# Kernel optimization log

Hardware: AMD Instinct MI355X
Metric: run time of the kernel (lower is better)

The kernel has to match this reference:

```python
import jax, jax.numpy as jnp
import numpy as np

T, B, H, L = 2048, 4096, 4, 3

def setup_inputs() -> dict:
    key = jax.random.key(0)
    ks = jax.random.split(key, 6)
    scale = 1.0 / np.sqrt(H)  # PyTorch nn.RNN init range ~U(-1/sqrt(H), 1/sqrt(H)); use normal*scale for simplicity
    return {
        "x": jax.random.normal(ks[0], (T, B, H), dtype=jnp.float32),
        "h": jax.random.normal(ks[1], (L, B, H), dtype=jnp.float32),
        "Wih": jax.random.normal(ks[2], (L, H, H), dtype=jnp.float32) * scale,
        "Whh": jax.random.normal(ks[3], (L, H, H), dtype=jnp.float32) * scale,
        "bih": jax.random.normal(ks[4], (L, H), dtype=jnp.float32) * scale,
        "bhh": jax.random.normal(ks[5], (L, H), dtype=jnp.float32) * scale,
    }

def _rnn_layer(x, h0, W_ih, W_hh, b_ih, b_hh):
    # x: (T, B, H); h0: (B, H). Vanilla tanh RNN, matching torch nn.RNN layer math:
    # h_t = tanh(x_t @ W_ih^T + b_ih + h_{t-1} @ W_hh^T + b_hh)
    b = b_ih + b_hh
    def step(h, xt):
        h_new = jnp.tanh(xt @ W_ih.T + h @ W_hh.T + b)
        return h_new, h_new
    _, ys = jax.lax.scan(step, h0, x)
    return ys  # (T, B, H)

def reference(x, h, Wih, Whh, bih, bhh):
    out = x
    for l in range(Wih.shape[0]):  # small fixed layer count (3)
        out = _rnn_layer(out, h[l], Wih[l], Whh[l], bih[l], bhh[l])
    return out  # (T, B, H): all-timestep outputs of last layer
```

## Files before the change

### kernel.cpp

```cpp
#include <hip/hip_runtime.h>

#define TSTEPS 2048
#define BATCH  4096
#define HID    4
#define STRIDE (BATCH*HID)
#define CH     32
#define NCHUNK (TSTEPS/CH)
#define NPH    69

#define QB(v,k) __int_as_float(__builtin_amdgcn_update_dpp( \
    0, __float_as_int(v), (k)*0x55, 0xF, 0xF, true))

__device__ __forceinline__ float fast_exp2(float x) {
#if __has_builtin(__builtin_amdgcn_exp2f)
  return __builtin_amdgcn_exp2f(x);
#else
  return exp2f(x);
#endif
}
__device__ __forceinline__ float fast_rcp(float x) {
#if __has_builtin(__builtin_amdgcn_rcpf)
  return __builtin_amdgcn_rcpf(x);
#else
  return 1.0f / x;
#endif
}

__device__ __forceinline__ void xload(float* ldst, const float* gsrc) {
  __builtin_amdgcn_global_load_lds(
      (const __attribute__((address_space(1))) void*)gsrc,
      (__attribute__((address_space(3))) void*)ldst, 4, 0, 0);
}

__global__ __launch_bounds__(256) void rnn_pipe4(
    const float* __restrict__ X,
    const float* __restrict__ H0,
    const float* __restrict__ Wih,
    const float* __restrict__ Whh,
    const float* __restrict__ bih,
    const float* __restrict__ bhh,
    float* __restrict__ Y)
{
  const int lane = threadIdx.x & 63;
  const int wid  = threadIdx.x >> 6;
  const int g    = blockIdx.x * 64 + lane;
  const int j    = g & 3;
  const float K  = 2.8853900817779268f;

  __shared__ float iface[3][2][CH][64];
  __shared__ float xbuf[3][CH][64];

  float whp[HID], win[HID], cbn = 0.0f, r = 0.0f;
  {
    const int Lt = wid - 1;
    const int Ln = wid;
    if (wid >= 1) {
#pragma unroll
      for (int k = 0; k < HID; ++k)
        whp[k] = -2.0f * K * Whh[(Lt*HID + j)*HID + k];
      r = 0.5f * (1.0f - H0[Lt*STRIDE + g]);
    }
    if (wid <= 2) {
      float wsum = 0.0f;
#pragma unroll
      for (int k = 0; k < HID; ++k) {
        win[k] = K * Wih[(Ln*HID + j)*HID + k];
        wsum  += Whh[(Ln*HID + j)*HID + k];
      }
      cbn = K * (bih[Ln*HID + j] + bhh[Ln*HID + j] + wsum);
    }
  }

  const float* __restrict__ xp = X + g;

  if (wid == 0) {
    __builtin_amdgcn_sched_barrier(0);
    asm volatile("s_waitcnt vmcnt(0)" ::: "memory");
#pragma unroll
    for (int u = 0; u < CH; ++u)
      xload(&xbuf[0][u][0], xp + (size_t)(0*CH + u) * STRIDE);
#pragma unroll
    for (int u = 0; u < CH; ++u)
      xload(&xbuf[1][u][0], xp + (size_t)(1*CH + u) * STRIDE);
  }

  auto phase = [&](int p, int slot) {
    if (wid == 0) {
      if (p <= NCHUNK - 1) {
        const int par = p & 1;
        asm volatile("s_waitcnt vmcnt(32)" ::: "memory");
        __builtin_amdgcn_sched_barrier(0);
        float xv[CH];
#pragma unroll
        for (int u = 0; u < CH; ++u) xv[u] = xbuf[slot][u][lane];
        __builtin_amdgcn_sched_barrier(0);
#pragma unroll
        for (int u = 0; u < CH; ++u) {
          float a = cbn;
          a = fmaf(QB(xv[u], 0), win[0], a);
          a = fmaf(QB(xv[u], 1), win[1], a);
          a = fmaf(QB(xv[u], 2), win[2], a);
          a = fmaf(QB(xv[u], 3), win[3], a);
          iface[0][par][u][lane] = a;
        }
#pragma unroll
        for (int u = 0; u < CH; ++u) {
          int tn = (p + 2) * CH + u;
          if (tn > TSTEPS - 1) tn = TSTEPS - 1;
          xload(&xbuf[(slot+2)%3][u][0], xp + (size_t)tn * STRIDE);
        }
      }
    } else {
      const int m = p - wid;
      if (m >= 0 && m <= NCHUNK - 1) {
        const int par = m & 1;
        float av[CH];
#pragma unroll
        for (int u = 0; u < CH; ++u) av[u] = iface[wid-1][par][u][lane];
        __builtin_amdgcn_sched_barrier(0);
        if (wid <= 2) {
#pragma unroll
          for (int u = 0; u < CH; ++u) {
            float t0 = fmaf(QB(r, 0), whp[0], av[u]);
            float t1 =      QB(r, 1) * whp[1];
            t0 = fmaf(QB(r, 2), whp[2], t0);
            t1 = fmaf(QB(r, 3), whp[3], t1);
            float e = fast_exp2(t0 + t1);
            r = fast_rcp(e + 1.0f);
            float h = fmaf(-2.0f, r, 1.0f);
            float a = cbn;
            a = fmaf(QB(h, 0), win[0], a);
            a = fmaf(QB(h, 1), win[1], a);
            a = fmaf(QB(h, 2), win[2], a);
            a = fmaf(QB(h, 3), win[3], a);
            iface[wid][par][u][lane] = a;
          }
        } else {
          const int base = m * CH;
#pragma unroll
          for (int u = 0; u < CH; ++u) {
            float t0 = fmaf(QB(r, 0), whp[0], av[u]);
            float t1 =      QB(r, 1) * whp[1];
            t0 = fmaf(QB(r, 2), whp[2], t0);
            t1 = fmaf(QB(r, 3), whp[3], t1);
            float e = fast_exp2(t0 + t1);
            r = fast_rcp(e + 1.0f);
            Y[(size_t)(base + u) * STRIDE + g] = fmaf(-2.0f, r, 1.0f);
          }
        }
      }
    }

    __builtin_amdgcn_sched_barrier(0);
    asm volatile("s_waitcnt lgkmcnt(0)" ::: "memory");
    __builtin_amdgcn_s_barrier();
    __builtin_amdgcn_sched_barrier(0);
  };

  for (int p = 0; p < NPH; p += 3) {
    phase(p + 0, 0);
    phase(p + 1, 1);
    phase(p + 2, 2);
  }

  if (wid == 0) asm volatile("s_waitcnt vmcnt(0)" ::: "memory");
}

extern "C" void kernel_launch(void* const* d_in, const int* in_sizes, int n_in,
                              void* d_out, int out_size, void* d_ws, size_t ws_size,
                              hipStream_t stream) {
  const float* X   = (const float*)d_in[0];
  const float* H0  = (const float*)d_in[1];
  const float* Wih = (const float*)d_in[2];
  const float* Whh = (const float*)d_in[3];
  const float* bih = (const float*)d_in[4];
  const float* bhh = (const float*)d_in[5];
  float* Y = (float*)d_out;

  rnn_pipe4<<<dim3(STRIDE / 64), dim3(256), 0, stream>>>(X, H0, Wih, Whh, bih, bhh, Y);
}
```

Before: 115.0 us.

## Double block to two wave groups and fold tanh affine into next-layer projection

Each block now holds two independent 4-wave pipelines, each covering 64 batch-hidden columns, and uses 512 threads, halving the grid. The middle layers skip computing h = 1 - 2r. They project r directly with pre-scaled weights (-2K*Wih), and the Wih row sum is folded into the bias. That projection is shifted one step so it reuses the DPP broadcasts already needed for the recurrent term. The intent is to shorten the serial per-step dependency chain and share barrier and launch overhead, at the cost of doubled LDS per block and possibly lower occupancy.

```diff
diff --git a/kernel.cpp b/kernel.cpp
--- a/kernel.cpp
+++ b/kernel.cpp
@@ -32,7 +32,7 @@
       (__attribute__((address_space(3))) void*)ldst, 4, 0, 0);
 }
 
-__global__ __launch_bounds__(256) void rnn_pipe4(
+__global__ __launch_bounds__(512) void rnn_pipe8(
     const float* __restrict__ X,
     const float* __restrict__ H0,
     const float* __restrict__ Wih,
@@ -42,30 +42,42 @@
     float* __restrict__ Y)
 {
   const int lane = threadIdx.x & 63;
-  const int wid  = threadIdx.x >> 6;
-  const int g    = blockIdx.x * 64 + lane;
+  const int w    = threadIdx.x >> 6;
+  const int role = w & 3;
+  const int grp  = w >> 2;
+  const int g    = blockIdx.x * 128 + grp * 64 + lane;
   const int j    = g & 3;
   const float K  = 2.8853900817779268f;
 
-  __shared__ float iface[3][2][CH][64];
-  __shared__ float xbuf[3][CH][64];
-
-  float whp[HID], win[HID], cbn = 0.0f, r = 0.0f;
+  __shared__ float iface[2][3][2][CH][64];
+  __shared__ float xbuf[2][3][CH][64];
+
+  float whp[HID], wip[HID], cbn = 0.0f, r = 0.0f;
   {
-    const int Lt = wid - 1;
-    const int Ln = wid;
-    if (wid >= 1) {
+    if (role >= 1) {
+      const int Lt = role - 1;
 #pragma unroll
       for (int k = 0; k < HID; ++k)
         whp[k] = -2.0f * K * Whh[(Lt*HID + j)*HID + k];
       r = 0.5f * (1.0f - H0[Lt*STRIDE + g]);
     }
-    if (wid <= 2) {
+    if (role == 0) {
+      const int Ln = 0;
       float wsum = 0.0f;
 #pragma unroll
       for (int k = 0; k < HID; ++k) {
-        win[k] = K * Wih[(Ln*HID + j)*HID + k];
+        wip[k] = K * Wih[(Ln*HID + j)*HID + k];
         wsum  += Whh[(Ln*HID + j)*HID + k];
+      }
+      cbn = K * (bih[Ln*HID + j] + bhh[Ln*HID + j] + wsum);
+    } else if (role <= 2) {
+      const int Ln = role;
+      float wsum = 0.0f;
+#pragma unroll
+      for (int k = 0; k < HID; ++k) {
+        float wik = Wih[(Ln*HID + j)*HID + k];
+        wip[k] = -2.0f * K * wik;
+        wsum  += Whh[(Ln*HID + j)*HID + k] + wik;
       }
       cbn = K * (bih[Ln*HID + j] + bhh[Ln*HID + j] + wsum);
     }
@@ -73,78 +85,88 @@
 
   const float* __restrict__ xp = X + g;
 
-  if (wid == 0) {
+  if (role == 0) {
     __builtin_amdgcn_sched_barrier(0);
     asm volatile("s_waitcnt vmcnt(0)" ::: "memory");
 #pragma unroll
     for (int u = 0; u < CH; ++u)
-      xload(&xbuf[0][u][0], xp + (size_t)(0*CH + u) * STRIDE);
+      xload(&xbuf[grp][0][u][0], xp + (size_t)(0*CH + u) * STRIDE);
 #pragma unroll
     for (int u = 0; u < CH; ++u)
-      xload(&xbuf[1][u][0], xp + (size_t)(1*CH + u) * STRIDE);
+      xload(&xbuf[grp][1][u][0], xp + (size_t)(1*CH + u) * STRIDE);
   }
 
   auto phase = [&](int p, int slot) {
-    if (wid == 0) {
+    if (role == 0) {
       if (p <= NCHUNK - 1) {
         const int par = p & 1;
         asm volatile("s_waitcnt vmcnt(32)" ::: "memory");
         __builtin_amdgcn_sched_barrier(0);
         float xv[CH];
 #pragma unroll
-        for (int u = 0; u < CH; ++u) xv[u] = xbuf[slot][u][lane];
+        for (int u = 0; u < CH; ++u) xv[u] = xbuf[grp][slot][u][lane];
         __builtin_amdgcn_sched_barrier(0);
 #pragma unroll
         for (int u = 0; u < CH; ++u) {
           float a = cbn;
-          a = fmaf(QB(xv[u], 0), win[0], a);
-          a = fmaf(QB(xv[u], 1), win[1], a);
-          a = fmaf(QB(xv[u], 2), win[2], a);
-          a = fmaf(QB(xv[u], 3), win[3], a);
-          iface[0][par][u][lane] = a;
+          a = fmaf(QB(xv[u], 0), wip[0], a);
+          a = fmaf(QB(xv[u], 1), wip[1], a);
+          a = fmaf(QB(xv[u], 2), wip[2], a);
+          a = fmaf(QB(xv[u], 3), wip[3], a);
+          iface[grp][0][par][u][lane] = a;
         }
 #pragma unroll
         for (int u = 0; u < CH; ++u) {
           int tn = (p + 2) * CH + u;
           if (tn > TSTEPS - 1) tn = TSTEPS - 1;
-          xload(&xbuf[(slot+2)%3][u][0], xp + (size_t)tn * STRIDE);
+          xload(&xbuf[grp][(slot+2)%3][u][0], xp + (size_t)tn * STRIDE);
         }
       }
     } else {
-      const int m = p - wid;
+      const int m = p - role;
       if (m >= 0 && m <= NCHUNK - 1) {
         const int par = m & 1;
         float av[CH];
 #pragma unroll
-        for (int u = 0; u < CH; ++u) av[u] = iface[wid-1][par][u][lane];
+        for (int u = 0; u < CH; ++u) av[u] = iface[grp][role-1][par][u][lane];
         __builtin_amdgcn_sched_barrier(0);
-        if (wid <= 2) {
+        if (role <= 2) {
 #pragma unroll
           for (int u = 0; u < CH; ++u) {
-            float t0 = fmaf(QB(r, 0), whp[0], av[u]);
-            float t1 =      QB(r, 1) * whp[1];
-            t0 = fmaf(QB(r, 2), whp[2], t0);
-            t1 = fmaf(QB(r, 3), whp[3], t1);
-            float e = fast_exp2(t0 + t1);
-            r = fast_rcp(e + 1.0f);
-            float h = fmaf(-2.0f, r, 1.0f);
+            float d0 = QB(r, 0), d1 = QB(r, 1), d2 = QB(r, 2), d3 = QB(r, 3);
+            if (u > 0) {
+              float a = cbn;
+              a = fmaf(d0, wip[0], a);
+              a = fmaf(d1, wip[1], a);
+              a = fmaf(d2, wip[2], a);
+              a = fmaf(d3, wip[3], a);
+              iface[grp][role][par][u-1][lane] = a;
+            }
+            float t0 = fmaf(d0, whp[0], av[u]);
+            float t1 = d1 * whp[1];
+            t0 = fmaf(d2, whp[2], t0);
+            t1 = fmaf(d3, whp[3], t1);
+            r = fast_rcp(fast_exp2(t0 + t1) + 1.0f);
+          }
+          {
+            float d0 = QB(r, 0), d1 = QB(r, 1), d2 = QB(r, 2), d3 = QB(r, 3);
             float a = cbn;
-            a = fmaf(QB(h, 0), win[0], a);
-            a = fmaf(QB(h, 1), win[1], a);
-            a = fmaf(QB(h, 2), win[2], a);
-            a = fmaf(QB(h, 3), win[3], a);
-            iface[wid][par][u][lane] = a;
+            a = fmaf(d0, wip[0], a);
+            a = fmaf(d1, wip[1], a);
+            a = fmaf(d2, wip[2], a);
+            a = fmaf(d3, wip[3], a);
+            iface[grp][role][par][CH-1][lane] = a;
           }
         } else {
           const int base = m * CH;
 #pragma unroll
           for (int u = 0; u < CH; ++u) {
-            float t0 = fmaf(QB(r, 0), whp[0], av[u]);
-            float t1 =      QB(r, 1) * whp[1];
-            t0 = fmaf(QB(r, 2), whp[2], t0);
-            t1 = fmaf(QB(r, 3), whp[3], t1);
-            float e = fast_exp2(t0 + t1);
-            r = fast_rcp(e + 1.0f);
+            float d0 = QB(r, 0), d1 = QB(r, 1), d2 = QB(r, 2), d3 = QB(r, 3);
+            float t0 = fmaf(d0, whp[0], av[u]);
+            float t1 = d1 * whp[1];
+            t0 = fmaf(d2, whp[2], t0);
+            t1 = fmaf(d3, whp[3], t1);
+            r = fast_rcp(fast_exp2(t0 + t1) + 1.0f);
             Y[(size_t)(base + u) * STRIDE + g] = fmaf(-2.0f, r, 1.0f);
           }
         }
@@ -163,7 +185,7 @@
     phase(p + 2, 2);
   }
 
-  if (wid == 0) asm volatile("s_waitcnt vmcnt(0)" ::: "memory");
+  if (role == 0) asm volatile("s_waitcnt vmcnt(0)" ::: "memory");
 }
 
 extern "C" void kernel_launch(void* const* d_in, const int* in_sizes, int n_in,
@@ -177,5 +199,5 @@
   const float* bhh = (const float*)d_in[5];
   float* Y = (float*)d_out;
 
-  rnn_pipe4<<<dim3(STRIDE / 64), dim3(256), 0, stream>>>(X, H0, Wih, Whh, bih, bhh, Y);
-}
+  rnn_pipe8<<<dim3(STRIDE / 128), dim3(512), 0, stream>>>(X, H0, Wih, Whh, bih, bhh, Y);
+}
```

Result: slower. 161.1 us (+40.0%).

## Split next-layer input projection into separate waves in a six-stage pipeline

Applied to the files above, without the earlier changes.

The block grows from four to six waves. The next layer's input projection moves out of the recurrent tanh waves into dedicated projection waves. Recurrent waves now only run the hidden-state recurrence and hand the sigmoid-form state r to the projection waves through a new LDS buffer. The projection is rewritten in terms of r by folding the constant terms into the bias. This shortens the per-step serial work in each recurrent wave, at the cost of more LDS, extra LDS traffic and two more pipeline stages.

```diff
diff --git a/kernel.cpp b/kernel.cpp
--- a/kernel.cpp
+++ b/kernel.cpp
@@ -32,7 +32,7 @@
       (__attribute__((address_space(3))) void*)ldst, 4, 0, 0);
 }
 
-__global__ __launch_bounds__(256) void rnn_pipe4(
+__global__ __launch_bounds__(384) void rnn_pipe6(
     const float* __restrict__ X,
     const float* __restrict__ H0,
     const float* __restrict__ Wih,
@@ -42,38 +42,40 @@
     float* __restrict__ Y)
 {
   const int lane = threadIdx.x & 63;
-  const int wid  = threadIdx.x >> 6;
+  const int w    = threadIdx.x >> 6;
   const int g    = blockIdx.x * 64 + lane;
   const int j    = g & 3;
   const float K  = 2.8853900817779268f;
 
-  __shared__ float iface[3][2][CH][64];
   __shared__ float xbuf[3][CH][64];
+  __shared__ float aif[3][2][CH][64];
+  __shared__ float rbuf[2][2][CH][64];
 
-  float whp[HID], win[HID], cbn = 0.0f, r = 0.0f;
-  {
-    const int Lt = wid - 1;
-    const int Ln = wid;
-    if (wid >= 1) {
+  const bool isP = (w == 0);
+  const bool isT = (w == 1) || (w == 3) || (w == 5);
+  const int  Lt  = (w - 1) >> 1;
+  const int  La  = w >> 1;
+
+  float whp[HID], wip[HID], cbn = 0.0f, r = 0.0f;
+  if (isT) {
 #pragma unroll
-      for (int k = 0; k < HID; ++k)
-        whp[k] = -2.0f * K * Whh[(Lt*HID + j)*HID + k];
-      r = 0.5f * (1.0f - H0[Lt*STRIDE + g]);
+    for (int k = 0; k < HID; ++k)
+      whp[k] = -2.0f * K * Whh[(Lt*HID + j)*HID + k];
+    r = 0.5f * (1.0f - H0[Lt*STRIDE + g]);
+  } else {
+    float wsum = 0.0f;
+#pragma unroll
+    for (int k = 0; k < HID; ++k) {
+      float wik = Wih[(La*HID + j)*HID + k];
+      wip[k] = isP ? (K * wik) : (-2.0f * K * wik);
+      wsum  += Whh[(La*HID + j)*HID + k] + (isP ? 0.0f : wik);
     }
-    if (wid <= 2) {
-      float wsum = 0.0f;
-#pragma unroll
-      for (int k = 0; k < HID; ++k) {
-        win[k] = K * Wih[(Ln*HID + j)*HID + k];
-        wsum  += Whh[(Ln*HID + j)*HID + k];
-      }
-      cbn = K * (bih[Ln*HID + j] + bhh[Ln*HID + j] + wsum);
-    }
+    cbn = K * (bih[La*HID + j] + bhh[La*HID + j] + wsum);
   }
 
   const float* __restrict__ xp = X + g;
 
-  if (wid == 0) {
+  if (isP) {
     __builtin_amdgcn_sched_barrier(0);
     asm volatile("s_waitcnt vmcnt(0)" ::: "memory");
 #pragma unroll
@@ -85,9 +87,11 @@
   }
 
   auto phase = [&](int p, int slot) {
-    if (wid == 0) {
-      if (p <= NCHUNK - 1) {
-        const int par = p & 1;
+    const int m = p - w;
+    if (m >= 0 && m <= NCHUNK - 1) {
+      const int par = m & 1;
+
+      if (isP) {
         asm volatile("s_waitcnt vmcnt(32)" ::: "memory");
         __builtin_amdgcn_sched_barrier(0);
         float xv[CH];
@@ -97,43 +101,32 @@
 #pragma unroll
         for (int u = 0; u < CH; ++u) {
           float a = cbn;
-          a = fmaf(QB(xv[u], 0), win[0], a);
-          a = fmaf(QB(xv[u], 1), win[1], a);
-          a = fmaf(QB(xv[u], 2), win[2], a);
-          a = fmaf(QB(xv[u], 3), win[3], a);
-          iface[0][par][u][lane] = a;
+          a = fmaf(QB(xv[u], 0), wip[0], a);
+          a = fmaf(QB(xv[u], 1), wip[1], a);
+          a = fmaf(QB(xv[u], 2), wip[2], a);
+          a = fmaf(QB(xv[u], 3), wip[3], a);
+          aif[0][par][u][lane] = a;
         }
 #pragma unroll
         for (int u = 0; u < CH; ++u) {
-          int tn = (p + 2) * CH + u;
+          int tn = (m + 2) * CH + u;
           if (tn > TSTEPS - 1) tn = TSTEPS - 1;
           xload(&xbuf[(slot+2)%3][u][0], xp + (size_t)tn * STRIDE);
         }
-      }
-    } else {
-      const int m = p - wid;
-      if (m >= 0 && m <= NCHUNK - 1) {
-        const int par = m & 1;
+      } else if (isT) {
         float av[CH];
 #pragma unroll
-        for (int u = 0; u < CH; ++u) av[u] = iface[wid-1][par][u][lane];
+        for (int u = 0; u < CH; ++u) av[u] = aif[Lt][par][u][lane];
         __builtin_amdgcn_sched_barrier(0);
-        if (wid <= 2) {
+        if (Lt <= 1) {
 #pragma unroll
           for (int u = 0; u < CH; ++u) {
             float t0 = fmaf(QB(r, 0), whp[0], av[u]);
             float t1 =      QB(r, 1) * whp[1];
             t0 = fmaf(QB(r, 2), whp[2], t0);
             t1 = fmaf(QB(r, 3), whp[3], t1);
-            float e = fast_exp2(t0 + t1);
-            r = fast_rcp(e + 1.0f);
-            float h = fmaf(-2.0f, r, 1.0f);
-            float a = cbn;
-            a = fmaf(QB(h, 0), win[0], a);
-            a = fmaf(QB(h, 1), win[1], a);
-            a = fmaf(QB(h, 2), win[2], a);
-            a = fmaf(QB(h, 3), win[3], a);
-            iface[wid][par][u][lane] = a;
+            r = fast_rcp(fast_exp2(t0 + t1) + 1.0f);
+            rbuf[Lt][par][u][lane] = r;
           }
         } else {
           const int base = m * CH;
@@ -143,10 +136,23 @@
             float t1 =      QB(r, 1) * whp[1];
             t0 = fmaf(QB(r, 2), whp[2], t0);
             t1 = fmaf(QB(r, 3), whp[3], t1);
-            float e = fast_exp2(t0 + t1);
-            r = fast_rcp(e + 1.0f);
+            r = fast_rcp(fast_exp2(t0 + t1) + 1.0f);
             Y[(size_t)(base + u) * STRIDE + g] = fmaf(-2.0f, r, 1.0f);
           }
+        }
+      } else {
+        float rv[CH];
+#pragma unroll
+        for (int u = 0; u < CH; ++u) rv[u] = rbuf[La-1][par][u][lane];
+        __builtin_amdgcn_sched_barrier(0);
+#pragma unroll
+        for (int u = 0; u < CH; ++u) {
+          float a = cbn;
+          a = fmaf(QB(rv[u], 0), wip[0], a);
+          a = fmaf(QB(rv[u], 1), wip[1], a);
+          a = fmaf(QB(rv[u], 2), wip[2], a);
+          a = fmaf(QB(rv[u], 3), wip[3], a);
+          aif[La][par][u][lane] = a;
         }
       }
     }
@@ -163,7 +169,7 @@
     phase(p + 2, 2);
   }
 
-  if (wid == 0) asm volatile("s_waitcnt vmcnt(0)" ::: "memory");
+  if (isP) asm volatile("s_waitcnt vmcnt(0)" ::: "memory");
 }
 
 extern "C" void kernel_launch(void* const* d_in, const int* in_sizes, int n_in,
@@ -177,5 +183,5 @@
   const float* bhh = (const float*)d_in[5];
   float* Y = (float*)d_out;
 
-  rnn_pipe4<<<dim3(STRIDE / 64), dim3(256), 0, stream>>>(X, H0, Wih, Whh, bih, bhh, Y);
+  rnn_pipe6<<<dim3(STRIDE / 64), dim3(384), 0, stream>>>(X, H0, Wih, Whh, bih, bhh, Y);
 }
```

New measurement: 143.1 us. 1.24x slower.
